# Kernel optimization log

Hardware: AMD Instinct MI355X
Metric: run time of the kernel (lower is better)

Reference implementation:

```python
import jax, jax.numpy as jnp
import numpy as np

B, N, K, IN_CH = 512, 64, 16, 6   # graphs, nodes per graph, knn, input features
EPS = 1e-5


def _w(key, shape, fan_in):
    return jax.random.normal(key, shape, jnp.float32) / np.sqrt(fan_in)


def setup_inputs() -> dict:
    key = jax.random.key(0)
    ks = jax.random.split(key, 16)
    f32 = jnp.float32
    inp = {
        "x": jax.random.normal(ks[0], (B * N, IN_CH), f32),
        "batch": (jnp.arange(B * N, dtype=jnp.int32) // N).astype(jnp.int32),
        # input projection 6 -> 64
        "w_in": _w(ks[1], (IN_CH, 64), IN_CH), "g_in": jnp.ones(64, f32), "b_in": jnp.zeros(64, f32),
        # ec1: SharedMLP([128, 64, 64])
        "w1a": _w(ks[2], (128, 64), 128), "g1a": jnp.ones(64, f32), "b1a": jnp.zeros(64, f32),
        "w1b": _w(ks[3], (64, 64), 64),   "g1b": jnp.ones(64, f32), "b1b": jnp.zeros(64, f32),
        # ec2: SharedMLP([128, 128, 128])
        "w2a": _w(ks[4], (128, 128), 128), "g2a": jnp.ones(128, f32), "b2a": jnp.zeros(128, f32),
        "w2b": _w(ks[5], (128, 128), 128), "g2b": jnp.ones(128, f32), "b2b": jnp.zeros(128, f32),
        # ec3: SharedMLP([256, 256, 256])
        "w3a": _w(ks[6], (256, 256), 256), "g3a": jnp.ones(256, f32), "b3a": jnp.zeros(256, f32),
        "w3b": _w(ks[7], (256, 256), 256), "g3b": jnp.ones(256, f32), "b3b": jnp.zeros(256, f32),
        # classifier head (dropout is identity in eval mode)
        "wc1": _w(ks[8], (896, 512), 896), "gc1": jnp.ones(512, f32), "bc1": jnp.zeros(512, f32),
        "wc2": _w(ks[9], (512, 256), 512), "gc2": jnp.ones(256, f32), "bc2": jnp.zeros(256, f32),
        "wc3": _w(ks[10], (256, 2), 256),  "bc3": jnp.zeros(2, f32),
    }
    return inp


def bn(h, g, b):
    # training-mode BatchNorm1d over all leading (node/edge) dims, biased var
    ax = tuple(range(h.ndim - 1))
    m = h.mean(ax)
    v = h.var(ax)
    return g * (h - m) * jax.lax.rsqrt(v + EPS) + b


def lrelu(h):
    return jax.nn.leaky_relu(h, 0.2)


def knn(x):
    # x: [B,N,C]; per-graph squared-Euclidean kNN (excluding self)
    sq = jnp.sum(x * x, -1)
    d = sq[:, :, None] - 2.0 * jnp.einsum('bnc,bmc->bnm', x, x) + sq[:, None, :]
    _, idx = jax.lax.top_k(-d, K + 1)  # K+1 smallest distances
    return idx[:, :, 1:]               # drop self -> [B,N,K]


def edge_conv(x, w1, g1, b1, w2, g2, b2):
    # Dynamic EdgeConv, aggr='max'. Edge (src=centre c, dst=neighbour n):
    # target x_i = x_n, message = MLP(cat[x_i, x_j - x_i]) with x_j = x_c.
    idx = knn(x)                                     # [B,N,K]
    xn = jax.vmap(lambda xb, ib: xb[ib])(x, idx)     # [B,N,K,C] neighbours
    xc = x[:, :, None, :]                            # centres broadcast
    feat = jnp.concatenate([xn, xc - xn], -1)        # [B,N,K,2C]
    h = lrelu(bn(feat @ w1, g1, b1))
    h = lrelu(bn(h @ w2, g2, b2))                    # [B,N,K,Cout]
    C = h.shape[-1]

    def scatter_max(ib, hb):  # per-graph max-scatter to destination nodes
        out = jnp.full((N, C), -jnp.inf, hb.dtype)
        return out.at[ib.reshape(-1)].max(hb.reshape(-1, C))

    res = jax.vmap(scatter_max)(idx, h)
    return jnp.where(jnp.isneginf(res), 0.0, res)    # nodes w/o in-edges -> 0


def reference(x, batch, w_in, g_in, b_in,
              w1a, g1a, b1a, w1b, g1b, b1b,
              w2a, g2a, b2a, w2b, g2b, b2b,
              w3a, g3a, b3a, w3b, g3b, b3b,
              wc1, gc1, bc1, wc2, gc2, bc2, wc3, bc3):
    # batch == arange(B*N)//N (equal-size graphs), encoded by the [B,N] reshape
    h0 = lrelu(bn(x @ w_in, g_in, b_in)).reshape(B, N, 64)
    h1 = edge_conv(h0, w1a, g1a, b1a, w1b, g1b, b1b)   # [B,N,64]
    h2 = edge_conv(h1, w2a, g2a, b2a, w2b, g2b, b2b)   # [B,N,128]
    h3 = edge_conv(h2, w3a, g3a, b3a, w3b, g3b, b3b)   # [B,N,256]
    h = jnp.concatenate([h1, h2, h3], -1)              # [B,N,448]
    pooled = jnp.concatenate([h.mean(1), h.max(1)], -1)  # [B,896]
    z = lrelu(bn(pooled @ wc1, gc1, bc1))
    z = lrelu(bn(z @ wc2, gc2, bc2))
    return z @ wc3 + bc3                               # [B,2] logits
```

## Files before the change

### kernel.cpp

```cpp
#include <hip/hip_runtime.h>
#include <hip/hip_fp16.h>
#include <math.h>

#define BB 512
#define NN 64
#define KNB 16
#define NPTS (BB*NN)
#define NEDGE (BB*NN*KNB)
#define EPSV 1e-5f

typedef __attribute__((ext_vector_type(8))) _Float16 f16x8;
typedef __attribute__((ext_vector_type(4))) _Float16 f16x4;
typedef __attribute__((ext_vector_type(4))) float f32x4;

__device__ __forceinline__ float lrelu(float x){ return x > 0.0f ? x : 0.2f*x; }
__device__ __forceinline__ unsigned encf(float f){
    unsigned u = __float_as_uint(f);
    return (u & 0x80000000u) ? ~u : (u | 0x80000000u);
}
__device__ __forceinline__ float decf(unsigned e){
    unsigned u = (e & 0x80000000u) ? (e ^ 0x80000000u) : ~e;
    return __uint_as_float(u);
}
#define ENC_NEGINF 0x007FFFFFu

__device__ __forceinline__ void split2h(float v, _Float16& h, _Float16& m){
    h = (_Float16)v;
    float r = v - (float)h;
    m = (_Float16)(r * 2048.0f);
}

__global__ void k_input(const float* __restrict__ x, const float* __restrict__ w,
                        float* __restrict__ h0){
    __shared__ float wls[6*64];
    int t = threadIdx.x;
    for (int i = t; i < 6*64; i += 256) wls[i] = w[i];
    __syncthreads();
    int row = blockIdx.x*256 + t;
    float xv[6];
#pragma unroll
    for (int k = 0; k < 6; k++) xv[k] = x[row*6 + k];
#pragma unroll 8
    for (int c = 0; c < 64; c++){
        float acc = 0.f;
#pragma unroll
        for (int k = 0; k < 6; k++) acc += xv[k]*wls[k*64 + c];
        h0[(size_t)row*64 + c] = acc;
    }
}

__global__ void k_colstats_part(const float* __restrict__ h,
                                float* __restrict__ pS, float* __restrict__ pQ){
    int t = threadIdx.x;
    int c = t & 63;
    int g = t >> 6;
    int p = blockIdx.x*4 + g;
    const int rpb = NPTS/256;
    int r0 = p*rpb;
    float s = 0.f, q = 0.f;
    for (int r = r0; r < r0 + rpb; r++){
        float v = h[(size_t)r*64 + c];
        s += v; q += v*v;
    }
    pS[c*256 + p] = s;
    pQ[c*256 + p] = q;
}

__global__ void k_bnfin_part(const float* __restrict__ pS, const float* __restrict__ pQ,
                             const float* __restrict__ g, const float* __restrict__ b,
                             float* __restrict__ cA, float* __restrict__ cB,
                             int P, float invM){
    int c = threadIdx.x;
    const float* ps = pS + (size_t)c*P;
    const float* pq = pQ + (size_t)c*P;
    float s = 0.f, q = 0.f;
    for (int p = 0; p < P; p += 4){
        float4 vs = *(const float4*)(ps + p);
        float4 vq = *(const float4*)(pq + p);
        s += vs.x + vs.y + vs.z + vs.w;
        q += vq.x + vq.y + vq.z + vq.w;
    }
    float m = s*invM;
    float v = q*invM - m*m;
    v = v < 0.f ? 0.f : v;
    float a = g[c]*rsqrtf(v + EPSV);
    cA[c] = a;
    cB[c] = b[c] - m*a;
}

__global__ void k_bnfin(const float* gs, const float* gq, const float* g,
                        const float* b, float* cA, float* cB, int C, float invM){
    int c = blockIdx.x*blockDim.x + threadIdx.x;
    if (c < C){
        float m = gs[c]*invM;
        float v = gq[c]*invM - m*m;
        v = v < 0.f ? 0.f : v;
        float a = g[c]*rsqrtf(v + EPSV);
        cA[c] = a;
        cB[c] = b[c] - m*a;
    }
}

__global__ void k_apply(float* h, const float* __restrict__ cA,
                        const float* __restrict__ cB, int C, int total){
    int i = blockIdx.x*256 + threadIdx.x;
    if (i < total){
        int c = i & (C-1);
        h[i] = lrelu(cA[c]*h[i] + cB[c]);
    }
}

template<int C>
__global__ void k_knn(const float* __restrict__ x, int* __restrict__ idxg){
    const int CP = C + 4;
    __shared__ __align__(16) float xls[64*CP];
    __shared__ float sq[64];
    __shared__ __align__(16) float dls[64*64];
    int t = threadIdx.x, b = blockIdx.x;
    const float* xb = x + (size_t)b*64*C;
    for (int i = t; i < 64*C; i += 256){
        int n = i / C, c = i & (C-1);
        xls[n*CP + c] = xb[i];
    }
    __syncthreads();
    if (t < 64){
        float s = 0.f;
        for (int c = 0; c < C; c += 4){
            float4 v = *(const float4*)&xls[t*CP + c];
            s += v.x*v.x + v.y*v.y + v.z*v.z + v.w*v.w;
        }
        sq[t] = s;
    }
    __syncthreads();
    {
        int n  = t >> 2;
        int m0 = (t & 3)*16;
        float acc[16];
#pragma unroll
        for (int i = 0; i < 16; i++) acc[i] = 0.f;
        const float* an = &xls[n*CP];
        const float* bm = &xls[m0*CP];
        for (int c = 0; c < C; c += 4){
            float4 a = *(const float4*)(an + c);
#pragma unroll
            for (int i = 0; i < 16; i++){
                float4 bv = *(const float4*)(bm + i*CP + c);
                acc[i] += a.x*bv.x + a.y*bv.y + a.z*bv.z + a.w*bv.w;
            }
        }
        float sn = sq[n];
#pragma unroll
        for (int i4 = 0; i4 < 16; i4 += 4){
            float4 dv;
            dv.x = sn - 2.0f*acc[i4+0] + sq[m0+i4+0];
            dv.y = sn - 2.0f*acc[i4+1] + sq[m0+i4+1];
            dv.z = sn - 2.0f*acc[i4+2] + sq[m0+i4+2];
            dv.w = sn - 2.0f*acc[i4+3] + sq[m0+i4+3];
            *(float4*)&dls[n*64 + m0 + i4] = dv;
        }
    }
    __syncthreads();
    int lane = t & 63, w = t >> 6;
    for (int pr = 0; pr < 16; pr += 4){
        int n0 = w*16 + pr;
        unsigned long long c0 = (((unsigned long long)encf(dls[(n0+0)*64 + lane])) << 32) | (unsigned)lane;
        unsigned long long c1 = (((unsigned long long)encf(dls[(n0+1)*64 + lane])) << 32) | (unsigned)lane;
        unsigned long long c2 = (((unsigned long long)encf(dls[(n0+2)*64 + lane])) << 32) | (unsigned)lane;
        unsigned long long c3 = (((unsigned long long)encf(dls[(n0+3)*64 + lane])) << 32) | (unsigned)lane;
#pragma unroll
        for (int k = 2; k <= 64; k <<= 1){
#pragma unroll
            for (int j = k >> 1; j > 0; j >>= 1){
                bool keepmin = ((lane & j) == 0) == ((lane & k) == 0);
                unsigned long long o0 = __shfl_xor(c0, j, 64);
                unsigned long long o1 = __shfl_xor(c1, j, 64);
                unsigned long long o2 = __shfl_xor(c2, j, 64);
                unsigned long long o3 = __shfl_xor(c3, j, 64);
                c0 = keepmin ? (c0 < o0 ? c0 : o0) : (c0 < o0 ? o0 : c0);
                c1 = keepmin ? (c1 < o1 ? c1 : o1) : (c1 < o1 ? o1 : c1);
                c2 = keepmin ? (c2 < o2 ? c2 : o2) : (c2 < o2 ? o2 : c2);
                c3 = keepmin ? (c3 < o3 ? c3 : o3) : (c3 < o3 ? o3 : c3);
            }
        }
        if (lane >= 1 && lane <= KNB){
            int base = b*1024 + n0*16 + lane - 1;
            idxg[base]      = (int)(c0 & 0xffffffffu);
            idxg[base + 16] = (int)(c1 & 0xffffffffu);
            idxg[base + 32] = (int)(c2 & 0xffffffffu);
            idxg[base + 48] = (int)(c3 & 0xffffffffu);
        }
    }
}

template<int CIN, int CMID, bool SPLIT>
__global__ void k_wprep(const float* __restrict__ w1,
                        _Float16* __restrict__ wbh, _Float16* __restrict__ wbm,
                        _Float16* __restrict__ wdh, _Float16* __restrict__ wdm){
    int i = blockIdx.x*256 + threadIdx.x;
    if (i >= CIN*CMID) return;
    int k = i / CMID, c = i - k*CMID;
    float wb = w1[(size_t)(CIN + k)*CMID + c];
    float wd = w1[(size_t)k*CMID + c] - wb;
    size_t o = (size_t)c*CIN + k;
    if (SPLIT){
        _Float16 h, m;
        split2h(wb, h, m); wbh[o] = h; wbm[o] = m;
        split2h(wd, h, m); wdh[o] = h; wdm[o] = m;
    } else {
        wbh[o] = (_Float16)wb;
        wdh[o] = (_Float16)wd;
    }
}

template<int CIN, int CMID>
__global__ __launch_bounds__(256)
void k_mm1x(const float* __restrict__ x,
            const _Float16* __restrict__ wbh, const _Float16* __restrict__ wbm,
            const _Float16* __restrict__ wdh, const _Float16* __restrict__ wdm,
            float* __restrict__ P, float* __restrict__ Q){
    int t = threadIdx.x, b = blockIdx.x;
    int lane = t & 63, w = t >> 6;
    int lrow = lane & 15, lk = lane >> 4;
    const int KT = CIN/32;
    f16x8 ah[KT], am[KT];
    {
        const float* xr = x + ((size_t)b*64 + w*16 + lrow)*CIN;
#pragma unroll
        for (int kt = 0; kt < KT; kt++){
            union { f16x8 v; _Float16 u[8]; } H, M;
#pragma unroll
            for (int j = 0; j < 8; j++)
                split2h(xr[kt*32 + lk*8 + j], H.u[j], M.u[j]);
            ah[kt] = H.v; am[kt] = M.v;
        }
    }
#pragma unroll
    for (int ct = 0; ct < CMID/16; ct++){
        int col = ct*16 + lrow;
        f32x4 aPM = {0,0,0,0}, aPC = {0,0,0,0};
        f32x4 aQM = {0,0,0,0}, aQC = {0,0,0,0};
#pragma unroll
        for (int kt = 0; kt < KT; kt++){
            size_t bo = (size_t)col*CIN + kt*32 + lk*8;
            f16x8 bbh = *(const f16x8*)(wbh + bo);
            f16x8 bbm = *(const f16x8*)(wbm + bo);
            f16x8 bdh = *(const f16x8*)(wdh + bo);
            f16x8 bdm = *(const f16x8*)(wdm + bo);
            aPM = __builtin_amdgcn_mfma_f32_16x16x32_f16(ah[kt], bbh, aPM, 0, 0, 0);
            aPC = __builtin_amdgcn_mfma_f32_16x16x32_f16(ah[kt], bbm, aPC, 0, 0, 0);
            aPC = __builtin_amdgcn_mfma_f32_16x16x32_f16(am[kt], bbh, aPC, 0, 0, 0);
            aQM = __builtin_amdgcn_mfma_f32_16x16x32_f16(ah[kt], bdh, aQM, 0, 0, 0);
            aQC = __builtin_amdgcn_mfma_f32_16x16x32_f16(ah[kt], bdm, aQC, 0, 0, 0);
            aQC = __builtin_amdgcn_mfma_f32_16x16x32_f16(am[kt], bdh, aQC, 0, 0, 0);
        }
#pragma unroll
        for (int u = 0; u < 4; u++){
            size_t o = ((size_t)b*64 + w*16 + lk*4 + u)*CMID + col;
            P[o] = aPM[u] + aPC[u]*(1.0f/2048.0f);
            Q[o] = aQM[u] + aQC[u]*(1.0f/2048.0f);
        }
    }
}

template<int CIN, int CMID>
__global__ __launch_bounds__(256)
void k_mm1xh(const float* __restrict__ x,
             const _Float16* __restrict__ wbh, const _Float16* __restrict__ wdh,
             _Float16* __restrict__ P, _Float16* __restrict__ Q){
    int t = threadIdx.x, b = blockIdx.x;
    int lane = t & 63, w = t >> 6;
    int lrow = lane & 15, lk = lane >> 4;
    const int KT = CIN/32;
    f16x8 ah[KT];
    {
        const float* xr = x + ((size_t)b*64 + w*16 + lrow)*CIN;
#pragma unroll
        for (int kt = 0; kt < KT; kt++){
            union { f16x8 v; _Float16 u[8]; } H;
#pragma unroll
            for (int j = 0; j < 8; j++)
                H.u[j] = (_Float16)xr[kt*32 + lk*8 + j];
            ah[kt] = H.v;
        }
    }
#pragma unroll
    for (int ct = 0; ct < CMID/16; ct++){
        int col = ct*16 + lrow;
        f32x4 aP = {0,0,0,0}, aQ = {0,0,0,0};
#pragma unroll
        for (int kt = 0; kt < KT; kt++){
            size_t bo = (size_t)col*CIN + kt*32 + lk*8;
            f16x8 bbh = *(const f16x8*)(wbh + bo);
            f16x8 bdh = *(const f16x8*)(wdh + bo);
            aP = __builtin_amdgcn_mfma_f32_16x16x32_f16(ah[kt], bbh, aP, 0, 0, 0);
            aQ = __builtin_amdgcn_mfma_f32_16x16x32_f16(ah[kt], bdh, aQ, 0, 0, 0);
        }
#pragma unroll
        for (int u = 0; u < 4; u++){
            size_t o = ((size_t)b*64 + w*16 + lk*4 + u)*CMID + col;
            P[o] = (_Float16)aP[u];
            Q[o] = (_Float16)aQ[u];
        }
    }
}

template<int CMID>
__global__ void k_stats1p(const float* __restrict__ P, const float* __restrict__ Q,
                          const int* __restrict__ idxg,
                          float* __restrict__ pS, float* __restrict__ pQ){
    int t = threadIdx.x, b = blockIdx.x;
    const int NG = 256/CMID;
    const int PT = 512*NG;
    int c = t & (CMID-1);
    int g = t / CMID;
    int epg = 1024/NG;
    const float* Pb = P + (size_t)b*64*CMID;
    const float* Qb = Q + (size_t)b*64*CMID;
    const int* ib = idxg + b*1024;
    float s = 0.f, q = 0.f;
    for (int e = g*epg; e < (g+1)*epg; e++){
        int n = e >> 4;
        int j = ib[e];
        float v = Pb[n*CMID + c] + Qb[j*CMID + c];
        s += v; q += v*v;
    }
    int p = b*NG + g;
    pS[(size_t)c*PT + p] = s;
    pQ[(size_t)c*PT + p] = q;
}

__global__ void k_stats1h(const _Float16* __restrict__ P, const _Float16* __restrict__ Q,
                          const int* __restrict__ idxg,
                          float* __restrict__ pS, float* __restrict__ pQ){
    __shared__ int ils[1024];
    int t = threadIdx.x, b = blockIdx.x;
    for (int i = t; i < 1024; i += 256) ils[i] = idxg[b*1024 + i];
    __syncthreads();
    const _Float16* Pb = P + (size_t)b*64*256;
    const _Float16* Qb = Q + (size_t)b*64*256;
    float s = 0.f, q = 0.f;
    for (int n = 0; n < 64; n++){
        float p = (float)Pb[n*256 + t];
#pragma unroll 4
        for (int k = 0; k < 16; k++){
            int j = ils[n*16 + k];
            float v = p + (float)Qb[j*256 + t];
            s += v; q += v*v;
        }
    }
    pS[(size_t)t*512 + b] = s;
    pQ[(size_t)t*512 + b] = q;
}

template<int CMID, int COUT, int NSET>
__global__ __launch_bounds__(256)
void k_mm2s(const float* __restrict__ P, const float* __restrict__ Q,
            const int* __restrict__ idxg,
            const float* __restrict__ cA1, const float* __restrict__ cB1,
            const float* __restrict__ w2, const float* __restrict__ g2,
            unsigned* __restrict__ outenc,
            float* __restrict__ pS, float* __restrict__ pQ){
    const int AS = CMID + 8;
    const int NCOL = 64*NSET;
    __shared__ __align__(16) _Float16 act_h[32*AS];
    __shared__ __align__(16) _Float16 act_m[32*AS];
    __shared__ unsigned maxtab[NCOL*65];
    __shared__ int ils[1024];
    __shared__ __align__(16) float a1ls[CMID];
    __shared__ __align__(16) float b1ls[CMID];
    int t = threadIdx.x, b = blockIdx.x, cc = blockIdx.y;
    int lane = t & 63, w = t >> 6;
    int lrow = lane & 15, lk = lane >> 4;

    for (int i = t; i < 1024; i += 256) ils[i] = idxg[b*1024 + i];
    for (int i = t; i < CMID; i += 256){ a1ls[i] = cA1[i]; b1ls[i] = cB1[i]; }
    for (int i = t; i < NCOL*65; i += 256) maxtab[i] = ENC_NEGINF;

    const int KT = CMID/32;
    f16x8 bh[NSET][KT], bm[NSET][KT];
    float sg[NSET];
    int ccBase = cc*NCOL;
#pragma unroll
    for (int s = 0; s < NSET; s++){
        int ncol = ccBase + s*64 + w*16 + lrow;
#pragma unroll
        for (int kt = 0; kt < KT; kt++){
            union { f16x8 v; _Float16 u[8]; } uh, um;
#pragma unroll
            for (int j = 0; j < 8; j++){
                int k = kt*32 + lk*8 + j;
                split2h(w2[(size_t)k*COUT + ncol], uh.u[j], um.u[j]);
            }
            bh[s][kt] = uh.v; bm[s][kt] = um.v;
        }
        sg[s] = (g2[ncol] < 0.0f) ? -1.0f : 1.0f;
    }
    float ss[NSET], qq[NSET];
#pragma unroll
    for (int s = 0; s < NSET; s++){ ss[s] = 0.f; qq[s] = 0.f; }
    const float* Pb = P + (size_t)b*64*CMID;
    const float* Qb = Q + (size_t)b*64*CMID;
    __syncthreads();

    for (int ch = 0; ch < 32; ch++){
        for (int i = t*4; i < 32*CMID; i += 1024){
            int le = i / CMID, k = i & (CMID-1);
            int e = ch*32 + le;
            int n = e >> 4, j = ils[e];
            float4 pv = *(const float4*)(Pb + n*CMID + k);
            float4 qv = *(const float4*)(Qb + j*CMID + k);
            float4 ca = *(const float4*)&a1ls[k];
            float4 cb = *(const float4*)&b1ls[k];
            float v0 = lrelu(ca.x*(pv.x + qv.x) + cb.x);
            float v1 = lrelu(ca.y*(pv.y + qv.y) + cb.y);
            float v2 = lrelu(ca.z*(pv.z + qv.z) + cb.z);
            float v3 = lrelu(ca.w*(pv.w + qv.w) + cb.w);
            union { f16x4 v; _Float16 u[4]; } hh, mm;
            split2h(v0, hh.u[0], mm.u[0]);
            split2h(v1, hh.u[1], mm.u[1]);
            split2h(v2, hh.u[2], mm.u[2]);
            split2h(v3, hh.u[3], mm.u[3]);
            *(f16x4*)&act_h[le*AS + k] = hh.v;
            *(f16x4*)&act_m[le*AS + k] = mm.v;
        }
        __syncthreads();

        f32x4 accM[2][NSET], accC[2][NSET];
#pragma unroll
        for (int r = 0; r < 2; r++)
#pragma unroll
            for (int s = 0; s < NSET; s++){
                accM[r][s] = {0.f,0.f,0.f,0.f};
                accC[r][s] = {0.f,0.f,0.f,0.f};
            }
#pragma unroll
        for (int kt = 0; kt < KT; kt++){
            int ko = kt*32 + lk*8;
#pragma unroll
            for (int r = 0; r < 2; r++){
                f16x8 ah = *(const f16x8*)&act_h[(r*16 + lrow)*AS + ko];
                f16x8 am = *(const f16x8*)&act_m[(r*16 + lrow)*AS + ko];
#pragma unroll
                for (int s = 0; s < NSET; s++){
                    accM[r][s] = __builtin_amdgcn_mfma_f32_16x16x32_f16(ah, bh[s][kt], accM[r][s], 0, 0, 0);
                    accC[r][s] = __builtin_amdgcn_mfma_f32_16x16x32_f16(ah, bm[s][kt], accC[r][s], 0, 0, 0);
                    accC[r][s] = __builtin_amdgcn_mfma_f32_16x16x32_f16(am, bh[s][kt], accC[r][s], 0, 0, 0);
                }
            }
        }
#pragma unroll
        for (int r = 0; r < 2; r++){
#pragma unroll
            for (int s = 0; s < NSET; s++){
#pragma unroll
                for (int u = 0; u < 4; u++){
                    int e = ch*32 + r*16 + lk*4 + u;
                    float v = accM[r][s][u] + accC[r][s][u]*(1.0f/2048.0f);
                    ss[s] += v; qq[s] += v*v;
                    int colL = s*64 + w*16 + lrow;
                    atomicMax(&maxtab[colL*65 + ils[e]], encf(sg[s]*v));
                }
            }
        }
        __syncthreads();
    }
#pragma unroll
    for (int s = 0; s < NSET; s++){
        ss[s] += __shfl_xor(ss[s], 16, 64); ss[s] += __shfl_xor(ss[s], 32, 64);
        qq[s] += __shfl_xor(qq[s], 16, 64); qq[s] += __shfl_xor(qq[s], 32, 64);
        if (lane < 16){
            pS[(size_t)(ccBase + s*64 + w*16 + lane)*512 + b] = ss[s];
            pQ[(size_t)(ccBase + s*64 + w*16 + lane)*512 + b] = qq[s];
        }
    }
    for (int i = t; i < 64*NCOL; i += 256){
        int colL = i % NCOL, j = i / NCOL;
        outenc[((size_t)b*64 + j)*COUT + ccBase + colL] = maxtab[colL*65 + j];
    }
}

template<int CMID, int COUT, int NSET>
__global__ __launch_bounds__(256)
void k_mm2xh(const _Float16* __restrict__ P, const _Float16* __restrict__ Q,
             const int* __restrict__ idxg,
             const float* __restrict__ cA1, const float* __restrict__ cB1,
             const float* __restrict__ w2, const float* __restrict__ g2,
             unsigned* __restrict__ outenc,
             float* __restrict__ pS, float* __restrict__ pQ){
    const int AS = CMID + 8;
    const int NCOL = 64*NSET;
    __shared__ __align__(16) _Float16 act[32*AS];
    __shared__ unsigned maxtab[NCOL*65];
    __shared__ int ils[1024];
    __shared__ __align__(16) _Float16 a1h[CMID];
    __shared__ __align__(16) _Float16 b1h[CMID];
    int t = threadIdx.x, b = blockIdx.x, cc = blockIdx.y;
    int lane = t & 63, w = t >> 6;
    int lrow = lane & 15, lk = lane >> 4;

    for (int i = t; i < 1024; i += 256) ils[i] = idxg[b*1024 + i];
    for (int i = t; i < CMID; i += 256){
        a1h[i] = (_Float16)cA1[i];
        b1h[i] = (_Float16)cB1[i];
    }
    for (int i = t; i < NCOL*65; i += 256) maxtab[i] = ENC_NEGINF;

    const int KT = CMID/32;
    f16x8 breg[NSET][KT];
    float sg[NSET];
    int ccBase = cc*NCOL;
#pragma unroll
    for (int s = 0; s < NSET; s++){
        int ncol = ccBase + s*64 + w*16 + lrow;
#pragma unroll
        for (int kt = 0; kt < KT; kt++){
            union { f16x8 v; _Float16 u[8]; } bu;
#pragma unroll
            for (int j = 0; j < 8; j++){
                int k = kt*32 + lk*8 + j;
                bu.u[j] = (_Float16)w2[(size_t)k*COUT + ncol];
            }
            breg[s][kt] = bu.v;
        }
        sg[s] = (g2[ncol] < 0.0f) ? -1.0f : 1.0f;
    }
    float ss[NSET], qq[NSET];
#pragma unroll
    for (int s = 0; s < NSET; s++){ ss[s] = 0.f; qq[s] = 0.f; }
    const _Float16* Pb = P + (size_t)b*64*CMID;
    const _Float16* Qb = Q + (size_t)b*64*CMID;
    __syncthreads();

    for (int ch = 0; ch < 32; ch++){
        for (int i = t*8; i < 32*CMID; i += 2048){
            int le = i / CMID, k = i & (CMID-1);
            int e = ch*32 + le;
            int n = e >> 4, j = ils[e];
            f16x8 pv = *(const f16x8*)(Pb + (size_t)n*CMID + k);
            f16x8 qv = *(const f16x8*)(Qb + (size_t)j*CMID + k);
            f16x8 ca = *(const f16x8*)&a1h[k];
            f16x8 cb = *(const f16x8*)&b1h[k];
            f16x8 v = ca*(pv + qv) + cb;
            f16x8 vm = v * (_Float16)0.2f;
            union { f16x8 x; _Float16 e8[8]; } V, M, R;
            V.x = v; M.x = vm;
#pragma unroll
            for (int u = 0; u < 8; u++)
                R.e8[u] = (V.e8[u] > (_Float16)0.0f) ? V.e8[u] : M.e8[u];
            *(f16x8*)&act[le*AS + k] = R.x;
        }
        __syncthreads();

        f32x4 acc[2][NSET];
#pragma unroll
        for (int r = 0; r < 2; r++)
#pragma unroll
            for (int s = 0; s < NSET; s++) acc[r][s] = {0.f,0.f,0.f,0.f};
#pragma unroll
        for (int kt = 0; kt < KT; kt++){
            int ko = kt*32 + lk*8;
#pragma unroll
            for (int r = 0; r < 2; r++){
                f16x8 a = *(const f16x8*)&act[(r*16 + lrow)*AS + ko];
#pragma unroll
                for (int s = 0; s < NSET; s++)
                    acc[r][s] = __builtin_amdgcn_mfma_f32_16x16x32_f16(a, breg[s][kt], acc[r][s], 0, 0, 0);
            }
        }
#pragma unroll
        for (int r = 0; r < 2; r++){
#pragma unroll
            for (int s = 0; s < NSET; s++){
#pragma unroll
                for (int u = 0; u < 4; u++){
                    int e = ch*32 + r*16 + lk*4 + u;
                    float v = acc[r][s][u];
                    ss[s] += v; qq[s] += v*v;
                    int colL = s*64 + w*16 + lrow;
                    atomicMax(&maxtab[colL*65 + ils[e]], encf(sg[s]*v));
                }
            }
        }
        __syncthreads();
    }
#pragma unroll
    for (int s = 0; s < NSET; s++){
        ss[s] += __shfl_xor(ss[s], 16, 64); ss[s] += __shfl_xor(ss[s], 32, 64);
        qq[s] += __shfl_xor(qq[s], 16, 64); qq[s] += __shfl_xor(qq[s], 32, 64);
        if (lane < 16){
            pS[(size_t)(ccBase + s*64 + w*16 + lane)*512 + b] = ss[s];
            pQ[(size_t)(ccBase + s*64 + w*16 + lane)*512 + b] = qq[s];
        }
    }
    for (int i = t; i < 64*NCOL; i += 256){
        int colL = i % NCOL, j = i / NCOL;
        outenc[((size_t)b*64 + j)*COUT + ccBase + colL] = maxtab[colL*65 + j];
    }
}

__global__ void k_final_ec(unsigned* __restrict__ buf, const float* __restrict__ cA,
                           const float* __restrict__ cB, const float* __restrict__ g,
                           int C, int total){
    int i = blockIdx.x*256 + threadIdx.x;
    if (i >= total) return;
    int c = i & (C-1);
    unsigned e = buf[i];
    float r;
    if (e == ENC_NEGINF) r = 0.0f;
    else {
        float s = (g[c] < 0.0f) ? -1.0f : 1.0f;
        float v = s*decf(e);
        r = lrelu(cA[c]*v + cB[c]);
    }
    ((float*)buf)[i] = r;
}

__global__ void k_pool(const float* __restrict__ h1, const float* __restrict__ h2,
                       const float* __restrict__ h3, float* __restrict__ pooled){
    int t = threadIdx.x, b = blockIdx.x;
    for (int c = t; c < 448; c += 256){
        const float* src; int C, cl;
        if (c < 64){ src = h1; C = 64;  cl = c; }
        else if (c < 192){ src = h2; C = 128; cl = c - 64; }
        else { src = h3; C = 256; cl = c - 192; }
        const float* p = src + (size_t)b*64*C + cl;
        float s = 0.f, mx = -INFINITY;
        for (int n = 0; n < 64; n++){
            float v = p[(size_t)n*C];
            s += v; mx = fmaxf(mx, v);
        }
        pooled[b*896 + c] = s*(1.0f/64.0f);
        pooled[b*896 + 448 + c] = mx;
    }
}

__global__ void k_fc1(const float* __restrict__ pooled, const float* __restrict__ w,
                      float* __restrict__ z, float* gs, float* gq){
    int r = blockIdx.x;
    int co = blockIdx.y*256 + threadIdx.x;
    const float* pr = pooled + r*896;
    float acc = 0.f;
    for (int k = 0; k < 896; k++) acc += pr[k]*w[(size_t)k*512 + co];
    z[(size_t)r*512 + co] = acc;
    atomicAdd(&gs[co], acc);
    atomicAdd(&gq[co], acc*acc);
}

__global__ void k_fc2(const float* __restrict__ z1, const float* __restrict__ cA,
                      const float* __restrict__ cB, const float* __restrict__ w,
                      float* __restrict__ z2, float* gs, float* gq){
    int r = blockIdx.x;
    int co = threadIdx.x;
    const float* zr = z1 + (size_t)r*512;
    float acc = 0.f;
    for (int k = 0; k < 512; k++){
        float v = lrelu(cA[k]*zr[k] + cB[k]);
        acc += v*w[(size_t)k*256 + co];
    }
    z2[(size_t)r*256 + co] = acc;
    atomicAdd(&gs[co], acc);
    atomicAdd(&gq[co], acc*acc);
}

__global__ void k_fc3(const float* __restrict__ z2, const float* __restrict__ cA,
                      const float* __restrict__ cB, const float* __restrict__ w,
                      const float* __restrict__ bias, float* __restrict__ out){
    int r = blockIdx.x*256 + threadIdx.x;
    const float* zr = z2 + (size_t)r*256;
    float a0 = 0.f, a1 = 0.f;
    for (int k = 0; k < 256; k++){
        float v = lrelu(cA[k]*zr[k] + cB[k]);
        a0 += v*w[k*2 + 0];
        a1 += v*w[k*2 + 1];
    }
    out[r*2 + 0] = a0 + bias[0];
    out[r*2 + 1] = a1 + bias[1];
}

extern "C" void kernel_launch(void* const* d_in, const int* in_sizes, int n_in,
                              void* d_out, int out_size, void* d_ws, size_t ws_size,
                              hipStream_t stream){
    const float* x    = (const float*)d_in[0];
    const float* w_in = (const float*)d_in[2];
    const float* g_in = (const float*)d_in[3];
    const float* b_in = (const float*)d_in[4];
    const float* w1a  = (const float*)d_in[5];
    const float* g1a  = (const float*)d_in[6];
    const float* b1a  = (const float*)d_in[7];
    const float* w1b  = (const float*)d_in[8];
    const float* g1b  = (const float*)d_in[9];
    const float* b1b  = (const float*)d_in[10];
    const float* w2a  = (const float*)d_in[11];
    const float* g2a  = (const float*)d_in[12];
    const float* b2a  = (const float*)d_in[13];
    const float* w2b  = (const float*)d_in[14];
    const float* g2b  = (const float*)d_in[15];
    const float* b2b  = (const float*)d_in[16];
    const float* w3a  = (const float*)d_in[17];
    const float* g3a  = (const float*)d_in[18];
    const float* b3a  = (const float*)d_in[19];
    const float* w3b  = (const float*)d_in[20];
    const float* g3b  = (const float*)d_in[21];
    const float* b3b  = (const float*)d_in[22];
    const float* wc1  = (const float*)d_in[23];
    const float* gc1  = (const float*)d_in[24];
    const float* bc1  = (const float*)d_in[25];
    const float* wc2  = (const float*)d_in[26];
    const float* gc2  = (const float*)d_in[27];
    const float* bc2  = (const float*)d_in[28];
    const float* wc3  = (const float*)d_in[29];
    const float* bc3  = (const float*)d_in[30];

    char* ws = (char*)d_ws;
    size_t off = 0;
    auto alloc = [&](size_t bytes){
        size_t o = off; off = (off + bytes + 255) & ~(size_t)255; return o;
    };
    float* h0     = (float*)(ws + alloc((size_t)NPTS*64*4));
    float* h1     = (float*)(ws + alloc((size_t)NPTS*64*4));
    float* h2     = (float*)(ws + alloc((size_t)NPTS*128*4));
    float* h3     = (float*)(ws + alloc((size_t)NPTS*256*4));
    float* P      = (float*)(ws + alloc((size_t)NPTS*256*4));
    float* Q      = (float*)(ws + alloc((size_t)NPTS*256*4));
    int*   idx    = (int*)  (ws + alloc((size_t)NPTS*16*4));
    float* pooled = (float*)(ws + alloc((size_t)512*896*4));
    float* z1     = (float*)(ws + alloc((size_t)512*512*4));
    float* z2     = (float*)(ws + alloc((size_t)512*256*4));
    float* pS     = (float*)(ws + alloc((size_t)131072*4));
    float* pQ     = (float*)(ws + alloc((size_t)131072*4));
    float* stats  = (float*)(ws + alloc((size_t)2048*4));
    float* coefs  = (float*)(ws + alloc((size_t)3456*4));
    _Float16* wsp = (_Float16*)(ws + alloc((size_t)114688*2));

    _Float16 *w1bh = wsp,          *w1bm = wsp+4096,
             *w1dh = wsp+8192,     *w1dm = wsp+12288;
    _Float16 *w2bh = wsp+16384,    *w2bm = wsp+24576,
             *w2dh = wsp+32768,    *w2dm = wsp+40960;
    _Float16 *w3bh = wsp+49152,    *w3dh = wsp+81920;

    float *f1s  = stats,       *f1q  = stats+512;
    float *f2s  = stats+1024,  *f2q  = stats+1280;
    float *cA0   = coefs,      *cB0   = coefs+64;
    float *cA1a  = coefs+128,  *cB1a  = coefs+192;
    float *cA1b  = coefs+256,  *cB1b  = coefs+320;
    float *cA2a  = coefs+384,  *cB2a  = coefs+512;
    float *cA2b  = coefs+640,  *cB2b  = coefs+768;
    float *cA3a  = coefs+896,  *cB3a  = coefs+1152;
    float *cA3b  = coefs+1408, *cB3b  = coefs+1664;
    float *cAf1  = coefs+1920, *cBf1  = coefs+2432;
    float *cAf2  = coefs+2944, *cBf2  = coefs+3200;

    (void)hipMemsetAsync(stats, 0, 2048*4, stream);

    k_wprep<64,64,true><<<16, 256, 0, stream>>>(w1a, w1bh, w1bm, w1dh, w1dm);
    k_wprep<64,128,true><<<32, 256, 0, stream>>>(w2a, w2bh, w2bm, w2dh, w2dm);
    k_wprep<128,256,false><<<128, 256, 0, stream>>>(w3a, w3bh, nullptr, w3dh, nullptr);

    k_input<<<NPTS/256, 256, 0, stream>>>(x, w_in, h0);
    k_colstats_part<<<64, 256, 0, stream>>>(h0, pS, pQ);
    k_bnfin_part<<<1, 64, 0, stream>>>(pS, pQ, g_in, b_in, cA0, cB0, 256, 1.0f/NPTS);
    k_apply<<<(NPTS*64)/256, 256, 0, stream>>>(h0, cA0, cB0, 64, NPTS*64);

    k_knn<64><<<BB, 256, 0, stream>>>(h0, idx);
    k_mm1x<64,64><<<BB, 256, 0, stream>>>(h0, w1bh, w1bm, w1dh, w1dm, P, Q);
    k_stats1p<64><<<BB, 256, 0, stream>>>(P, Q, idx, pS, pQ);
    k_bnfin_part<<<1, 64, 0, stream>>>(pS, pQ, g1a, b1a, cA1a, cB1a, 2048, 1.0f/NEDGE);
    k_mm2s<64,64,1><<<dim3(BB,1), 256, 0, stream>>>(P, Q, idx, cA1a, cB1a, w1b, g1b,
                                                    (unsigned*)h1, pS, pQ);
    k_bnfin_part<<<1, 64, 0, stream>>>(pS, pQ, g1b, b1b, cA1b, cB1b, 512, 1.0f/NEDGE);
    k_final_ec<<<(NPTS*64)/256, 256, 0, stream>>>((unsigned*)h1, cA1b, cB1b, g1b, 64, NPTS*64);

    k_knn<64><<<BB, 256, 0, stream>>>(h1, idx);
    k_mm1x<64,128><<<BB, 256, 0, stream>>>(h1, w2bh, w2bm, w2dh, w2dm, P, Q);
    k_stats1p<128><<<BB, 256, 0, stream>>>(P, Q, idx, pS, pQ);
    k_bnfin_part<<<1, 128, 0, stream>>>(pS, pQ, g2a, b2a, cA2a, cB2a, 1024, 1.0f/NEDGE);
    k_mm2s<128,128,2><<<dim3(BB,1), 256, 0, stream>>>(P, Q, idx, cA2a, cB2a, w2b, g2b,
                                                      (unsigned*)h2, pS, pQ);
    k_bnfin_part<<<1, 128, 0, stream>>>(pS, pQ, g2b, b2b, cA2b, cB2b, 512, 1.0f/NEDGE);
    k_final_ec<<<(NPTS*128)/256, 256, 0, stream>>>((unsigned*)h2, cA2b, cB2b, g2b, 128, NPTS*128);

    k_knn<128><<<BB, 256, 0, stream>>>(h2, idx);
    k_mm1xh<128,256><<<BB, 256, 0, stream>>>(h2, w3bh, w3dh, (_Float16*)P, (_Float16*)Q);
    k_stats1h<<<BB, 256, 0, stream>>>((_Float16*)P, (_Float16*)Q, idx, pS, pQ);
    k_bnfin_part<<<1, 256, 0, stream>>>(pS, pQ, g3a, b3a, cA3a, cB3a, 512, 1.0f/NEDGE);
    k_mm2xh<256,256,2><<<dim3(BB,2), 256, 0, stream>>>((_Float16*)P, (_Float16*)Q, idx,
                                                       cA3a, cB3a, w3b, g3b,
                                                       (unsigned*)h3, pS, pQ);
    k_bnfin_part<<<1, 256, 0, stream>>>(pS, pQ, g3b, b3b, cA3b, cB3b, 512, 1.0f/NEDGE);
    k_final_ec<<<(NPTS*256)/256, 256, 0, stream>>>((unsigned*)h3, cA3b, cB3b, g3b, 256, NPTS*256);

    k_pool<<<BB, 256, 0, stream>>>(h1, h2, h3, pooled);
    k_fc1<<<dim3(512,2), 256, 0, stream>>>(pooled, wc1, z1, f1s, f1q);
    k_bnfin<<<2, 256, 0, stream>>>(f1s, f1q, gc1, bc1, cAf1, cBf1, 512, 1.0f/512);
    k_fc2<<<512, 256, 0, stream>>>(z1, cAf1, cBf1, wc2, z2, f2s, f2q);
    k_bnfin<<<1, 256, 0, stream>>>(f2s, f2q, gc2, bc2, cAf2, cBf2, 256, 1.0f/512);
    k_fc3<<<2, 256, 0, stream>>>(z2, cAf2, cBf2, wc3, bc3, (float*)d_out);

    (void)in_sizes; (void)n_in; (void)out_size; (void)ws_size;
}
```

Before: 1.234 ms.

## Fuse BN-decode into consumers and co-launch kNN with first matmul

Removes the three k_final_ec passes. The encoded max-scatter outputs are now decoded with the BN/lrelu affine inside the consumers (kNN, first edge-conv matmul, pooling). The kNN and first-matmul kernels of each edge-conv stage are merged into one launch, with blockIdx.y selecting the role, so the two independent workloads run concurrently. This saves a full read and write of each feature map and several launches. In exchange each consumer redoes the decode, and the mm1x path decodes with scattered per-element loads of cA/cB/g.

```diff
diff --git a/kernel.cpp b/kernel.cpp
--- a/kernel.cpp
+++ b/kernel.cpp
@@ -23,6 +23,12 @@
     return __uint_as_float(u);
 }
 #define ENC_NEGINF 0x007FFFFFu
+
+__device__ __forceinline__ float dec_h(unsigned e, float ca, float cb, float gv){
+    if (e == ENC_NEGINF) return 0.0f;
+    float sgn = (gv < 0.0f) ? -1.0f : 1.0f;
+    return lrelu(ca*(sgn*decf(e)) + cb);
+}
 
 __device__ __forceinline__ void split2h(float v, _Float16& h, _Float16& m){
     h = (_Float16)v;
@@ -110,17 +116,28 @@
     }
 }
 
-template<int C>
-__global__ void k_knn(const float* __restrict__ x, int* __restrict__ idxg){
+template<int C, bool DEC>
+__device__ void knn_body(char* smemraw, const float* __restrict__ xf,
+                         const unsigned* __restrict__ xe,
+                         const float* __restrict__ cA, const float* __restrict__ cB,
+                         const float* __restrict__ g,
+                         int* __restrict__ idxg, int b, int t){
     const int CP = C + 4;
-    __shared__ __align__(16) float xls[64*CP];
-    __shared__ float sq[64];
-    __shared__ __align__(16) float dls[64*64];
-    int t = threadIdx.x, b = blockIdx.x;
-    const float* xb = x + (size_t)b*64*C;
-    for (int i = t; i < 64*C; i += 256){
-        int n = i / C, c = i & (C-1);
-        xls[n*CP + c] = xb[i];
+    float* xls = (float*)smemraw;
+    float* sq  = xls + 64*CP;
+    float* dls = sq + 64;
+    if (DEC){
+        const unsigned* xb = xe + (size_t)b*64*C;
+        for (int i = t; i < 64*C; i += 256){
+            int n = i / C, c = i - n*C;
+            xls[n*CP + c] = dec_h(xb[i], cA[c], cB[c], g[c]);
+        }
+    } else {
+        const float* xb = xf + (size_t)b*64*C;
+        for (int i = t; i < 64*C; i += 256){
+            int n = i / C, c = i - n*C;
+            xls[n*CP + c] = xb[i];
+        }
     }
     __syncthreads();
     if (t < 64){
@@ -212,25 +229,28 @@
     }
 }
 
-template<int CIN, int CMID>
-__global__ __launch_bounds__(256)
-void k_mm1x(const float* __restrict__ x,
-            const _Float16* __restrict__ wbh, const _Float16* __restrict__ wbm,
-            const _Float16* __restrict__ wdh, const _Float16* __restrict__ wdm,
-            float* __restrict__ P, float* __restrict__ Q){
-    int t = threadIdx.x, b = blockIdx.x;
+template<int CIN, int CMID, bool DEC>
+__device__ void mm1x_body(const float* __restrict__ xf, const unsigned* __restrict__ xe,
+                          const float* __restrict__ cA, const float* __restrict__ cB,
+                          const float* __restrict__ g,
+                          const _Float16* __restrict__ wbh, const _Float16* __restrict__ wbm,
+                          const _Float16* __restrict__ wdh, const _Float16* __restrict__ wdm,
+                          float* __restrict__ P, float* __restrict__ Q, int b, int t){
     int lane = t & 63, w = t >> 6;
     int lrow = lane & 15, lk = lane >> 4;
     const int KT = CIN/32;
     f16x8 ah[KT], am[KT];
     {
-        const float* xr = x + ((size_t)b*64 + w*16 + lrow)*CIN;
+        size_t ro = ((size_t)b*64 + w*16 + lrow)*CIN;
 #pragma unroll
         for (int kt = 0; kt < KT; kt++){
             union { f16x8 v; _Float16 u[8]; } H, M;
 #pragma unroll
-            for (int j = 0; j < 8; j++)
-                split2h(xr[kt*32 + lk*8 + j], H.u[j], M.u[j]);
+            for (int j = 0; j < 8; j++){
+                int k = kt*32 + lk*8 + j;
+                float xv = DEC ? dec_h(xe[ro + k], cA[k], cB[k], g[k]) : xf[ro + k];
+                split2h(xv, H.u[j], M.u[j]);
+            }
             ah[kt] = H.v; am[kt] = M.v;
         }
     }
@@ -262,24 +282,27 @@
     }
 }
 
-template<int CIN, int CMID>
-__global__ __launch_bounds__(256)
-void k_mm1xh(const float* __restrict__ x,
-             const _Float16* __restrict__ wbh, const _Float16* __restrict__ wdh,
-             _Float16* __restrict__ P, _Float16* __restrict__ Q){
-    int t = threadIdx.x, b = blockIdx.x;
+template<int CIN, int CMID, bool DEC>
+__device__ void mm1xh_body(const float* __restrict__ xf, const unsigned* __restrict__ xe,
+                           const float* __restrict__ cA, const float* __restrict__ cB,
+                           const float* __restrict__ g,
+                           const _Float16* __restrict__ wbh, const _Float16* __restrict__ wdh,
+                           _Float16* __restrict__ P, _Float16* __restrict__ Q, int b, int t){
     int lane = t & 63, w = t >> 6;
     int lrow = lane & 15, lk = lane >> 4;
     const int KT = CIN/32;
     f16x8 ah[KT];
     {
-        const float* xr = x + ((size_t)b*64 + w*16 + lrow)*CIN;
+        size_t ro = ((size_t)b*64 + w*16 + lrow)*CIN;
 #pragma unroll
         for (int kt = 0; kt < KT; kt++){
             union { f16x8 v; _Float16 u[8]; } H;
 #pragma unroll
-            for (int j = 0; j < 8; j++)
-                H.u[j] = (_Float16)xr[kt*32 + lk*8 + j];
+            for (int j = 0; j < 8; j++){
+                int k = kt*32 + lk*8 + j;
+                float xv = DEC ? dec_h(xe[ro + k], cA[k], cB[k], g[k]) : xf[ro + k];
+                H.u[j] = (_Float16)xv;
+            }
             ah[kt] = H.v;
         }
     }
@@ -302,6 +325,51 @@
             Q[o] = (_Float16)aQ[u];
         }
     }
+}
+
+__global__ __launch_bounds__(256)
+void k_s1(const float* __restrict__ h0,
+          const _Float16* wbh, const _Float16* wbm,
+          const _Float16* wdh, const _Float16* wdm,
+          int* __restrict__ idx, float* __restrict__ P, float* __restrict__ Q){
+    __shared__ __align__(16) char smem[(64*68 + 64 + 64*64)*4];
+    if (blockIdx.y == 0)
+        knn_body<64,false>(smem, h0, nullptr, nullptr, nullptr, nullptr,
+                           idx, blockIdx.x, threadIdx.x);
+    else
+        mm1x_body<64,64,false>(h0, nullptr, nullptr, nullptr, nullptr,
+                               wbh, wbm, wdh, wdm, P, Q, blockIdx.x, threadIdx.x);
+}
+
+__global__ __launch_bounds__(256)
+void k_s2(const unsigned* __restrict__ h1e,
+          const float* __restrict__ cA, const float* __restrict__ cB,
+          const float* __restrict__ g,
+          const _Float16* wbh, const _Float16* wbm,
+          const _Float16* wdh, const _Float16* wdm,
+          int* __restrict__ idx, float* __restrict__ P, float* __restrict__ Q){
+    __shared__ __align__(16) char smem[(64*68 + 64 + 64*64)*4];
+    if (blockIdx.y == 0)
+        knn_body<64,true>(smem, nullptr, h1e, cA, cB, g,
+                          idx, blockIdx.x, threadIdx.x);
+    else
+        mm1x_body<64,128,true>(nullptr, h1e, cA, cB, g,
+                               wbh, wbm, wdh, wdm, P, Q, blockIdx.x, threadIdx.x);
+}
+
+__global__ __launch_bounds__(256)
+void k_s3(const unsigned* __restrict__ h2e,
+          const float* __restrict__ cA, const float* __restrict__ cB,
+          const float* __restrict__ g,
+          const _Float16* wbh, const _Float16* wdh,
+          int* __restrict__ idx, _Float16* __restrict__ P, _Float16* __restrict__ Q){
+    __shared__ __align__(16) char smem[(64*132 + 64 + 64*64)*4];
+    if (blockIdx.y == 0)
+        knn_body<128,true>(smem, nullptr, h2e, cA, cB, g,
+                           idx, blockIdx.x, threadIdx.x);
+    else
+        mm1xh_body<128,256,true>(nullptr, h2e, cA, cB, g,
+                                 wbh, wdh, P, Q, blockIdx.x, threadIdx.x);
 }
 
 template<int CMID>
@@ -598,35 +666,28 @@
     }
 }
 
-__global__ void k_final_ec(unsigned* __restrict__ buf, const float* __restrict__ cA,
-                           const float* __restrict__ cB, const float* __restrict__ g,
-                           int C, int total){
-    int i = blockIdx.x*256 + threadIdx.x;
-    if (i >= total) return;
-    int c = i & (C-1);
-    unsigned e = buf[i];
-    float r;
-    if (e == ENC_NEGINF) r = 0.0f;
-    else {
-        float s = (g[c] < 0.0f) ? -1.0f : 1.0f;
-        float v = s*decf(e);
-        r = lrelu(cA[c]*v + cB[c]);
-    }
-    ((float*)buf)[i] = r;
-}
-
-__global__ void k_pool(const float* __restrict__ h1, const float* __restrict__ h2,
-                       const float* __restrict__ h3, float* __restrict__ pooled){
+__global__ void k_pool(const unsigned* __restrict__ h1e,
+                       const float* __restrict__ cA1, const float* __restrict__ cB1,
+                       const float* __restrict__ g1,
+                       const unsigned* __restrict__ h2e,
+                       const float* __restrict__ cA2, const float* __restrict__ cB2,
+                       const float* __restrict__ g2,
+                       const unsigned* __restrict__ h3e,
+                       const float* __restrict__ cA3, const float* __restrict__ cB3,
+                       const float* __restrict__ g3,
+                       float* __restrict__ pooled){
     int t = threadIdx.x, b = blockIdx.x;
     for (int c = t; c < 448; c += 256){
-        const float* src; int C, cl;
-        if (c < 64){ src = h1; C = 64;  cl = c; }
-        else if (c < 192){ src = h2; C = 128; cl = c - 64; }
-        else { src = h3; C = 256; cl = c - 192; }
-        const float* p = src + (size_t)b*64*C + cl;
+        const unsigned* src; int C, cl;
+        const float *cA, *cB, *g;
+        if (c < 64){ src = h1e; C = 64;  cl = c;       cA = cA1; cB = cB1; g = g1; }
+        else if (c < 192){ src = h2e; C = 128; cl = c - 64;  cA = cA2; cB = cB2; g = g2; }
+        else { src = h3e; C = 256; cl = c - 192; cA = cA3; cB = cB3; g = g3; }
+        float ca = cA[cl], cb = cB[cl], gv = g[cl];
+        const unsigned* p = src + (size_t)b*64*C + cl;
         float s = 0.f, mx = -INFINITY;
         for (int n = 0; n < 64; n++){
-            float v = p[(size_t)n*C];
+            float v = dec_h(p[(size_t)n*C], ca, cb, gv);
             s += v; mx = fmaxf(mx, v);
         }
         pooled[b*896 + c] = s*(1.0f/64.0f);
@@ -761,35 +822,33 @@
     k_bnfin_part<<<1, 64, 0, stream>>>(pS, pQ, g_in, b_in, cA0, cB0, 256, 1.0f/NPTS);
     k_apply<<<(NPTS*64)/256, 256, 0, stream>>>(h0, cA0, cB0, 64, NPTS*64);
 
-    k_knn<64><<<BB, 256, 0, stream>>>(h0, idx);
-    k_mm1x<64,64><<<BB, 256, 0, stream>>>(h0, w1bh, w1bm, w1dh, w1dm, P, Q);
+    k_s1<<<dim3(BB,2), 256, 0, stream>>>(h0, w1bh, w1bm, w1dh, w1dm, idx, P, Q);
     k_stats1p<64><<<BB, 256, 0, stream>>>(P, Q, idx, pS, pQ);
     k_bnfin_part<<<1, 64, 0, stream>>>(pS, pQ, g1a, b1a, cA1a, cB1a, 2048, 1.0f/NEDGE);
     k_mm2s<64,64,1><<<dim3(BB,1), 256, 0, stream>>>(P, Q, idx, cA1a, cB1a, w1b, g1b,
                                                     (unsigned*)h1, pS, pQ);
     k_bnfin_part<<<1, 64, 0, stream>>>(pS, pQ, g1b, b1b, cA1b, cB1b, 512, 1.0f/NEDGE);
-    k_final_ec<<<(NPTS*64)/256, 256, 0, stream>>>((unsigned*)h1, cA1b, cB1b, g1b, 64, NPTS*64);
-
-    k_knn<64><<<BB, 256, 0, stream>>>(h1, idx);
-    k_mm1x<64,128><<<BB, 256, 0, stream>>>(h1, w2bh, w2bm, w2dh, w2dm, P, Q);
+
+    k_s2<<<dim3(BB,2), 256, 0, stream>>>((const unsigned*)h1, cA1b, cB1b, g1b,
+                                         w2bh, w2bm, w2dh, w2dm, idx, P, Q);
     k_stats1p<128><<<BB, 256, 0, stream>>>(P, Q, idx, pS, pQ);
     k_bnfin_part<<<1, 128, 0, stream>>>(pS, pQ, g2a, b2a, cA2a, cB2a, 1024, 1.0f/NEDGE);
     k_mm2s<128,128,2><<<dim3(BB,1), 256, 0, stream>>>(P, Q, idx, cA2a, cB2a, w2b, g2b,
                                                       (unsigned*)h2, pS, pQ);
     k_bnfin_part<<<1, 128, 0, stream>>>(pS, pQ, g2b, b2b, cA2b, cB2b, 512, 1.0f/NEDGE);
-    k_final_ec<<<(NPTS*128)/256, 256, 0, stream>>>((unsigned*)h2, cA2b, cB2b, g2b, 128, NPTS*128);
-
-    k_knn<128><<<BB, 256, 0, stream>>>(h2, idx);
-    k_mm1xh<128,256><<<BB, 256, 0, stream>>>(h2, w3bh, w3dh, (_Float16*)P, (_Float16*)Q);
+
+    k_s3<<<dim3(BB,2), 256, 0, stream>>>((const unsigned*)h2, cA2b, cB2b, g2b,
+                                         w3bh, w3dh, idx, (_Float16*)P, (_Float16*)Q);
     k_stats1h<<<BB, 256, 0, stream>>>((_Float16*)P, (_Float16*)Q, idx, pS, pQ);
     k_bnfin_part<<<1, 256, 0, stream>>>(pS, pQ, g3a, b3a, cA3a, cB3a, 512, 1.0f/NEDGE);
     k_mm2xh<256,256,2><<<dim3(BB,2), 256, 0, stream>>>((_Float16*)P, (_Float16*)Q, idx,
                                                        cA3a, cB3a, w3b, g3b,
                                                        (unsigned*)h3, pS, pQ);
     k_bnfin_part<<<1, 256, 0, stream>>>(pS, pQ, g3b, b3b, cA3b, cB3b, 512, 1.0f/NEDGE);
-    k_final_ec<<<(NPTS*256)/256, 256, 0, stream>>>((unsigned*)h3, cA3b, cB3b, g3b, 256, NPTS*256);
-
-    k_pool<<<BB, 256, 0, stream>>>(h1, h2, h3, pooled);
+
+    k_pool<<<BB, 256, 0, stream>>>((const unsigned*)h1, cA1b, cB1b, g1b,
+                                   (const unsigned*)h2, cA2b, cB2b, g2b,
+                                   (const unsigned*)h3, cA3b, cB3b, g3b, pooled);
     k_fc1<<<dim3(512,2), 256, 0, stream>>>(pooled, wc1, z1, f1s, f1q);
     k_bnfin<<<2, 256, 0, stream>>>(f1s, f1q, gc1, bc1, cAf1, cBf1, 512, 1.0f/512);
     k_fc2<<<512, 256, 0, stream>>>(z1, cAf1, cBf1, wc2, z2, f2s, f2q);
```

Result: slower. 1.265 ms (+2.5%).
